# Kernel optimization log

Measured on AMD Instinct MI355X. Metric: run time of the kernel, lower is better.

The kernel has to match this reference:

```python
import jax, jax.numpy as jnp
import numpy as np
import math

B, HW, E = 128, 3136, 96
NH, WS = 3, 7
EH = E // NH
NEG_INF = float('-inf')


def setup_inputs() -> dict:
    key = jax.random.key(0)
    ks = jax.random.split(key, 5)
    x = jax.random.normal(ks[0], (B, HW, E), dtype=jnp.float32)
    w1 = jax.random.normal(ks[1], (3 * E, E), dtype=jnp.float32) * 0.02
    b1 = jnp.zeros((3 * E,), dtype=jnp.float32)
    w2 = jax.random.normal(ks[2], (E, E), dtype=jnp.float32) * 0.02
    b2 = jnp.zeros((E,), dtype=jnp.float32)
    return {"x": x, "w1": w1, "b1": b1, "w2": w2, "b2": b2}


def _masks():
    m = WS * (WS // 2)  # 21
    row = jnp.zeros((WS * WS, WS * WS), dtype=jnp.float32)
    row = row.at[-m:, :-m].set(NEG_INF)
    row = row.at[:-m, -m:].set(NEG_INF)
    # rearrange '(r w1) (c w2) -> (w1 r) (w2 c)'
    col = row.reshape(WS, WS, WS, WS).transpose(1, 0, 3, 2).reshape(WS * WS, WS * WS)
    return row, col


def reference(x, w1, b1, w2, b2):
    b = x.shape[0]
    hh = ww = int(round(math.sqrt(x.shape[1])))
    nh, nw = hh // WS, ww // WS
    qkv = x @ w1.T + b1                      # [b, hw, 3E]
    qkv = qkv.reshape(b, hh, ww, E, 3)       # (c K) split, K=3
    # cyclic shift: (-WS)//2 == -4 (faithful to torch source)
    s = (-WS) // 2
    qkv = jnp.roll(qkv, (s, s), axis=(1, 2))
    # window partition: b (h m1) (w m2) (H E) K -> b H h w (m1 m2) E K
    t = qkv.reshape(b, nh, WS, nw, WS, NH, EH, 3)
    t = t.transpose(0, 5, 1, 3, 2, 4, 6, 7).reshape(b, NH, nh, nw, WS * WS, EH, 3)
    q, k, v = t[..., 0], t[..., 1], t[..., 2]
    att = jnp.einsum('bHxyqe,bHxyke->bHxyqk', q, k) / math.sqrt(EH)
    row_mask, col_mask = _masks()
    att = att.at[:, :, -1, :].add(row_mask)
    att = att.at[:, :, :, -1].add(col_mask)
    p = jax.nn.softmax(att, axis=-1)
    o = jnp.einsum('bHxyqk,bHxyke->bHxyqe', p, v)
    # reverse window partition: b H h w (m1 m2) E -> b (h m1) (w m2) (H E)
    o = o.reshape(b, NH, nh, nw, WS, WS, EH)
    o = o.transpose(0, 2, 4, 3, 5, 1, 6).reshape(b, hh, ww, E)
    o = jnp.roll(o, (WS // 2, WS // 2), axis=(1, 2))  # +3 (faithful)
    o = o.reshape(b, hh * ww, E)
    return o @ w2.T + b2
```

## Files before the change

kernel.cpp:

```cpp
#include <hip/hip_runtime.h>

typedef __attribute__((ext_vector_type(8))) __bf16 bf16x8;
typedef __attribute__((ext_vector_type(4))) float f32x4;
typedef __attribute__((ext_vector_type(4))) unsigned int u32x4;

__device__ __forceinline__ unsigned short f2bf(float f){
    unsigned int x = __builtin_bit_cast(unsigned int, f);
    x += 0x7FFFu + ((x >> 16) & 1u);
    return (unsigned short)(x >> 16);
}
__device__ __forceinline__ unsigned int pk2(float a, float b){
    return (unsigned int)f2bf(a) | ((unsigned int)f2bf(b) << 16);
}
__device__ __forceinline__ bf16x8 ldfrag(const unsigned short* p){
    u32x4 v = *reinterpret_cast<const u32x4*>(p);
    return __builtin_bit_cast(bf16x8, v);
}
__device__ __forceinline__ bf16x8 ldf32(const float* p){
    f32x4 a = *reinterpret_cast<const f32x4*>(p);
    f32x4 b = *reinterpret_cast<const f32x4*>(p + 4);
    u32x4 r;
    r[0] = pk2(a[0], a[1]); r[1] = pk2(a[2], a[3]);
    r[2] = pk2(b[0], b[1]); r[3] = pk2(b[2], b[3]);
    return __builtin_bit_cast(bf16x8, r);
}
__device__ __forceinline__ f32x4 mfma_bf16(bf16x8 a, bf16x8 b, f32x4 c){
    return __builtin_amdgcn_mfma_f32_16x16x32_bf16(a, b, c, 0, 0, 0);
}

#define W1F_SH 27648
#define W2F_SH 9216

__global__ __launch_bounds__(256) void k_prep(const float* __restrict__ w1,
                                              const float* __restrict__ b1,
                                              const float* __restrict__ w2,
                                              unsigned short* __restrict__ w1f,
                                              unsigned short* __restrict__ w2f,
                                              float* __restrict__ b1p)
{
    int i = blockIdx.x * 256 + threadIdx.x;
    if (i < 3456){
        int f = i >> 6, lane = i & 63;
        int n = f / 3, ks = f - n * 3;
        int l15 = lane & 15, qd = lane >> 4;
        int rp = n * 16 + l15;
        int c = rp / 96, rem = rp - c * 96;
        const float* src = w1 + (size_t)(3 * rem + c) * 96 + ks * 32 + qd * 8;
        f32x4 v0 = *reinterpret_cast<const f32x4*>(src);
        f32x4 v1 = *reinterpret_cast<const f32x4*>(src + 4);
        u32x4 p;
        p[0] = pk2(v0[0], v0[1]); p[1] = pk2(v0[2], v0[3]);
        p[2] = pk2(v1[0], v1[1]); p[3] = pk2(v1[2], v1[3]);
        *reinterpret_cast<u32x4*>(w1f + (size_t)f * 512 + lane * 8) = p;
    } else if (i < 4608){
        int j = i - 3456;
        int f = j >> 6, lane = j & 63;
        int n = f / 3, ks = f - n * 3;
        int l15 = lane & 15, qd = lane >> 4;
        const float* src = w2 + (size_t)(n * 16 + l15) * 96 + ks * 32 + qd * 8;
        f32x4 v0 = *reinterpret_cast<const f32x4*>(src);
        f32x4 v1 = *reinterpret_cast<const f32x4*>(src + 4);
        u32x4 p;
        p[0] = pk2(v0[0], v0[1]); p[1] = pk2(v0[2], v0[3]);
        p[2] = pk2(v1[0], v1[1]); p[3] = pk2(v1[2], v1[3]);
        *reinterpret_cast<u32x4*>(w2f + (size_t)f * 512 + lane * 8) = p;
    } else if (i < 4896){
        int rp = i - 4608;
        int c = rp / 96, rem = rp - c * 96;
        b1p[rp] = b1[3 * rem + c];
    }
}

__global__ __launch_bounds__(256, 4) void k_fused(const float* __restrict__ x,
                                                  const unsigned short* __restrict__ w1f,
                                                  const float* __restrict__ b1p,
                                                  const unsigned short* __restrict__ w2f,
                                                  const float* __restrict__ b2,
                                                  float* __restrict__ out)
{
    __shared__ __align__(16) unsigned short smem[19200];
    unsigned short* Qr = smem;
    unsigned short* Kr = smem + 6144;
    unsigned short* Vt = smem + 12288;
    unsigned short* o_lds = smem;
    float* o2 = reinterpret_cast<float*>(smem + 6144);

    const int tid = threadIdx.x;
    const int win = blockIdx.x;
    const int b = win >> 6, wy = (win >> 3) & 7, wx = win & 7;
    const int wave = tid >> 6, lane = tid & 63;
    const int l15 = lane & 15, qd = lane >> 4;

    {
        int pos = wave * 16 + l15;
        int iy = pos / 7, ix = pos - iy * 7;
        int h = wy * 7 + iy + 4; if (h >= 56) h -= 56;
        int w = wx * 7 + ix + 4; if (w >= 56) w -= 56;
        const float* xr = x + ((size_t)b * 3136 + h * 56 + w) * 96 + qd * 8;
        bf16x8 aX0 = ldf32(xr);
        bf16x8 aX1 = ldf32(xr + 32);
        bf16x8 aX2 = ldf32(xr + 64);

        f32x4 acc[18];
#pragma unroll
        for (int n = 0; n < 18; ++n){
            const unsigned short* wf = w1f + (size_t)(n * 3) * 512 + lane * 8;
            f32x4 a = {0.f, 0.f, 0.f, 0.f};
            a = mfma_bf16(aX0, ldfrag(wf), a);
            a = mfma_bf16(aX1, ldfrag(wf + 512), a);
            a = mfma_bf16(aX2, ldfrag(wf + 1024), a);
            acc[n] = a;
        }
        float bias[18];
#pragma unroll
        for (int n = 0; n < 18; ++n) bias[n] = b1p[n * 16 + l15];

#pragma unroll
        for (int n = 0; n < 18; ++n){
            if (n < 12){
                int c = n / 6, H = (n % 6) >> 1;
                int eh = ((n & 1) << 4) + l15;
                int ch = eh >> 3;
                unsigned short* base = (c == 0 ? Qr : Kr) + H * 2048;
#pragma unroll
                for (int r = 0; r < 4; ++r){
                    int p = wave * 16 + qd * 4 + r;
                    int chs = ch ^ ((p >> 1) & 3);
                    base[p * 32 + chs * 8 + (eh & 7)] = f2bf(acc[n][r] + bias[n]);
                }
            } else {
                int H = (n - 12) >> 1;
                int eh = ((n & 1) << 4) + l15;
#pragma unroll
                for (int r = 0; r < 4; ++r){
                    int p = wave * 16 + qd * 4 + r;
                    Vt[(H * 32 + eh) * 72 + p] = f2bf(acc[n][r] + bias[n]);
                }
            }
        }
    }
    __syncthreads();

    const bool rowm = (wy == 7), colm = (wx == 7);
    const float scale = 0.17677669529663687f;
    const float NEGINF = -__builtin_inff();

    unsigned int m49 = 0, m28 = 0, m7 = 0;
#pragma unroll
    for (int tn = 0; tn < 4; ++tn)
#pragma unroll
        for (int r = 0; r < 4; ++r){
            int col = tn * 16 + qd * 4 + r;
            int bit = tn * 4 + r;
            m49 |= (unsigned)(col >= 49) << bit;
            m28 |= (unsigned)(col >= 28) << bit;
            m7  |= (unsigned)((col % 7) >= 4) << bit;
        }
    const int src0 = l15 + 16 * ((2 * qd) & 3);
    const int src1 = l15 + 16 * ((2 * qd + 1) & 3);
    const int chq = qd ^ ((l15 >> 1) & 3);

    for (int u = 0; u < 3; ++u){
        int unit = wave * 3 + u;
        int H = unit >> 2, tm = unit & 3;
        int qrow = tm * 16 + l15;
        bool rhi = (qrow >= 28);
        bool rc7 = ((qrow % 7) >= 4);

        bf16x8 bQ = ldfrag(Qr + H * 2048 + (tm * 16 + l15) * 32 + chq * 8);
        f32x4 S[4];
#pragma unroll
        for (int tn = 0; tn < 4; ++tn){
            bf16x8 aK = ldfrag(Kr + H * 2048 + (tn * 16 + l15) * 32 + chq * 8);
            f32x4 z = {0.f, 0.f, 0.f, 0.f};
            S[tn] = mfma_bf16(aK, bQ, z);
        }

        float mx = NEGINF;
#pragma unroll
        for (int tn = 0; tn < 4; ++tn)
#pragma unroll
            for (int r = 0; r < 4; ++r){
                int bit = tn * 4 + r;
                float v = S[tn][r] * scale;
                bool blocked = (((m49 >> bit) & 1u) != 0u)
                    || (rowm && (rhi != (((m28 >> bit) & 1u) != 0u)))
                    || (colm && (rc7 != (((m7 >> bit) & 1u) != 0u)));
                v = blocked ? NEGINF : v;
                S[tn][r] = v;
                mx = fmaxf(mx, v);
            }
        mx = fmaxf(mx, __shfl_xor(mx, 16, 64));
        mx = fmaxf(mx, __shfl_xor(mx, 32, 64));
        float sum = 0.f;
#pragma unroll
        for (int tn = 0; tn < 4; ++tn)
#pragma unroll
            for (int r = 0; r < 4; ++r){
                float e = exp2f((S[tn][r] - mx) * 1.4426950408889634f);
                S[tn][r] = e;
                sum += e;
            }
        sum += __shfl_xor(sum, 16, 64);
        sum += __shfl_xor(sum, 32, 64);
        float inv = 1.f / sum;

        unsigned int pkv[8];
#pragma unroll
        for (int tn = 0; tn < 4; ++tn){
            pkv[tn * 2]     = pk2(S[tn][0], S[tn][1]);
            pkv[tn * 2 + 1] = pk2(S[tn][2], S[tn][3]);
        }

        f32x4 O[2];
        O[0] = (f32x4){0.f, 0.f, 0.f, 0.f};
        O[1] = (f32x4){0.f, 0.f, 0.f, 0.f};
#pragma unroll
        for (int kt = 0; kt < 2; ++kt){
            u32x4 aw;
#pragma unroll
            for (int w4 = 0; w4 < 4; ++w4){
                int srcl = (w4 < 2) ? src0 : src1;
                unsigned int lo = (unsigned int)__shfl((int)pkv[(2 * kt) * 2 + (w4 & 1)], srcl, 64);
                unsigned int hi = (unsigned int)__shfl((int)pkv[(2 * kt + 1) * 2 + (w4 & 1)], srcl, 64);
                aw[w4] = (qd >= 2) ? hi : lo;
            }
            bf16x8 aP = __builtin_bit_cast(bf16x8, aw);
#pragma unroll
            for (int tn = 0; tn < 2; ++tn){
                bf16x8 bV = ldfrag(Vt + (H * 32 + tn * 16 + l15) * 72 + kt * 32 + qd * 8);
                O[tn] = mfma_bf16(aP, bV, O[tn]);
            }
        }

#pragma unroll
        for (int r = 0; r < 4; ++r){
            float invr = __shfl(inv, qd * 4 + r, 64);
            int p = tm * 16 + qd * 4 + r;
            int swz = (p >> 1) & 3;
#pragma unroll
            for (int tn = 0; tn < 2; ++tn){
                int eh = tn * 16 + l15;
                int chs = (eh >> 3) ^ swz;
                o_lds[(H * 64 + p) * 32 + chs * 8 + (eh & 7)] = f2bf(O[tn][r] * invr);
            }
        }
    }
    __syncthreads();

    {
        int prow = wave * 16 + l15;
        bf16x8 a0 = ldfrag(o_lds + (0 * 64 + prow) * 32 + chq * 8);
        bf16x8 a1 = ldfrag(o_lds + (1 * 64 + prow) * 32 + chq * 8);
        bf16x8 a2 = ldfrag(o_lds + (2 * 64 + prow) * 32 + chq * 8);
#pragma unroll
        for (int n = 0; n < 6; ++n){
            const unsigned short* wf = w2f + (size_t)(n * 3) * 512 + lane * 8;
            f32x4 a = {0.f, 0.f, 0.f, 0.f};
            a = mfma_bf16(a0, ldfrag(wf), a);
            a = mfma_bf16(a1, ldfrag(wf + 512), a);
            a = mfma_bf16(a2, ldfrag(wf + 1024), a);
            float bias2 = b2[n * 16 + l15];
#pragma unroll
            for (int r = 0; r < 4; ++r)
                o2[(wave * 16 + qd * 4 + r) * 100 + n * 16 + l15] = a[r] + bias2;
        }
    }
    __syncthreads();

    {
        int row = tid >> 2, seg = tid & 3;
        if (row < 49){
            int iy = row / 7, ix = row - iy * 7;
            int h = wy * 7 + iy + 3; if (h >= 56) h -= 56;
            int w = wx * 7 + ix + 3; if (w >= 56) w -= 56;
            const float* src = o2 + row * 100 + seg * 24;
            float* dst = out + ((size_t)b * 3136 + h * 56 + w) * 96 + seg * 24;
#pragma unroll
            for (int v = 0; v < 6; ++v){
                f32x4 t4;
#pragma unroll
                for (int j = 0; j < 4; ++j) t4[j] = src[v * 4 + j];
                *reinterpret_cast<f32x4*>(dst + v * 4) = t4;
            }
        }
    }
}

extern "C" void kernel_launch(void* const* d_in, const int* in_sizes, int n_in,
                              void* d_out, int out_size, void* d_ws, size_t ws_size,
                              hipStream_t stream)
{
    const float* x  = (const float*)d_in[0];
    const float* w1 = (const float*)d_in[1];
    const float* b1 = (const float*)d_in[2];
    const float* w2 = (const float*)d_in[3];
    const float* b2 = (const float*)d_in[4];
    float* out = (float*)d_out;

    unsigned short* w1f = (unsigned short*)d_ws;
    unsigned short* w2f = w1f + W1F_SH;
    float* b1p = (float*)(w2f + W2F_SH);

    hipLaunchKernelGGL(k_prep,  dim3(20),   dim3(256), 0, stream, w1, b1, w2, w1f, w2f, b1p);
    hipLaunchKernelGGL(k_fused, dim3(8192), dim3(256), 0, stream, x, w1f, b1p, w2f, b2, out);
}
```

Before: 382.3 us.

## Keep Q, P and O in registers using 16x16x16 MFMA layouts

```diff
diff --git a/kernel.cpp b/kernel.cpp
--- a/kernel.cpp
+++ b/kernel.cpp
@@ -1,8 +1,10 @@
 #include <hip/hip_runtime.h>
 
 typedef __attribute__((ext_vector_type(8))) __bf16 bf16x8;
+typedef __attribute__((ext_vector_type(4))) short short4v;
 typedef __attribute__((ext_vector_type(4))) float f32x4;
 typedef __attribute__((ext_vector_type(4))) unsigned int u32x4;
+typedef __attribute__((ext_vector_type(2))) unsigned int u32x2;
 
 __device__ __forceinline__ unsigned short f2bf(float f){
     unsigned int x = __builtin_bit_cast(unsigned int, f);
@@ -28,62 +30,98 @@
     return __builtin_amdgcn_mfma_f32_16x16x32_bf16(a, b, c, 0, 0, 0);
 }
 
-#define W1F_SH 27648
-#define W2F_SH 9216
+#if defined(__has_builtin)
+#if __has_builtin(__builtin_amdgcn_mfma_f32_16x16x16bf16_1k)
+#define HAVE_MFMA16 1
+#endif
+#endif
+__device__ __forceinline__ f32x4 mfma16(short4v a, short4v b, f32x4 c){
+#ifdef HAVE_MFMA16
+    return __builtin_amdgcn_mfma_f32_16x16x16bf16_1k(a, b, c, 0, 0, 0);
+#else
+    f32x4 d;
+    asm volatile("s_nop 1\n\tv_mfma_f32_16x16x16_bf16 %0, %1, %2, %3\n\ts_nop 7\n\ts_nop 7"
+                 : "=v"(d) : "v"(a), "v"(b), "v"(c));
+    return d;
+#endif
+}
+
+#define VSTR 72
 
 __global__ __launch_bounds__(256) void k_prep(const float* __restrict__ w1,
                                               const float* __restrict__ b1,
                                               const float* __restrict__ w2,
-                                              unsigned short* __restrict__ w1f,
-                                              unsigned short* __restrict__ w2f,
-                                              float* __restrict__ b1p)
+                                              unsigned short* __restrict__ w1k,
+                                              unsigned short* __restrict__ w1v,
+                                              unsigned short* __restrict__ w1q,
+                                              unsigned short* __restrict__ w2p,
+                                              float* __restrict__ bias3)
 {
+    const float SCALE = 0.17677669529663687f;
     int i = blockIdx.x * 256 + threadIdx.x;
-    if (i < 3456){
-        int f = i >> 6, lane = i & 63;
+    if (i < 2304){
+        int half = i / 1152;
+        int j = i - half * 1152;
+        int f = j >> 6, lane = j & 63;
         int n = f / 3, ks = f - n * 3;
         int l15 = lane & 15, qd = lane >> 4;
-        int rp = n * 16 + l15;
-        int c = rp / 96, rem = rp - c * 96;
-        const float* src = w1 + (size_t)(3 * rem + c) * 96 + ks * 32 + qd * 8;
+        int row = 3 * (n * 16 + l15) + 1 + half;
+        const float* src = w1 + (size_t)row * 96 + ks * 32 + qd * 8;
         f32x4 v0 = *reinterpret_cast<const f32x4*>(src);
         f32x4 v1 = *reinterpret_cast<const f32x4*>(src + 4);
         u32x4 p;
         p[0] = pk2(v0[0], v0[1]); p[1] = pk2(v0[2], v0[3]);
         p[2] = pk2(v1[0], v1[1]); p[3] = pk2(v1[2], v1[3]);
-        *reinterpret_cast<u32x4*>(w1f + (size_t)f * 512 + lane * 8) = p;
+        unsigned short* dst = (half ? w1v : w1k) + (size_t)f * 512 + lane * 8;
+        *reinterpret_cast<u32x4*>(dst) = p;
     } else if (i < 4608){
-        int j = i - 3456;
+        int j = i - 2304;
         int f = j >> 6, lane = j & 63;
-        int n = f / 3, ks = f - n * 3;
+        int qt = f / 6, ks = f - qt * 6;
         int l15 = lane & 15, qd = lane >> 4;
-        const float* src = w2 + (size_t)(n * 16 + l15) * 96 + ks * 32 + qd * 8;
-        f32x4 v0 = *reinterpret_cast<const f32x4*>(src);
-        f32x4 v1 = *reinterpret_cast<const f32x4*>(src + 4);
-        u32x4 p;
-        p[0] = pk2(v0[0], v0[1]); p[1] = pk2(v0[2], v0[3]);
-        p[2] = pk2(v1[0], v1[1]); p[3] = pk2(v1[2], v1[3]);
-        *reinterpret_cast<u32x4*>(w2f + (size_t)f * 512 + lane * 8) = p;
-    } else if (i < 4896){
-        int rp = i - 4608;
-        int c = rp / 96, rem = rp - c * 96;
-        b1p[rp] = b1[3 * rem + c];
+        int row = 3 * (qt * 16 + l15);
+        const float* src = w1 + (size_t)row * 96 + ks * 16 + qd * 4;
+        f32x4 v = *reinterpret_cast<const f32x4*>(src);
+        u32x2 p;
+        p[0] = pk2(v[0] * SCALE, v[1] * SCALE);
+        p[1] = pk2(v[2] * SCALE, v[3] * SCALE);
+        *reinterpret_cast<u32x2*>(w1q + (size_t)(qt * 3 + (ks >> 1)) * 512 + lane * 8 + (ks & 1) * 4) = p;
+    } else if (i < 6912){
+        int j = i - 4608;
+        int f = j >> 6, lane = j & 63;
+        int n = f / 6, ct = f - n * 6;
+        int l15 = lane & 15, qd = lane >> 4;
+        const float* src = w2 + (size_t)(n * 16 + l15) * 96 + ct * 16 + qd * 4;
+        f32x4 v = *reinterpret_cast<const f32x4*>(src);
+        u32x2 p;
+        p[0] = pk2(v[0], v[1]); p[1] = pk2(v[2], v[3]);
+        *reinterpret_cast<u32x2*>(w2p + (size_t)(n * 3 + (ct >> 1)) * 512 + lane * 8 + (ct & 1) * 4) = p;
+    } else if (i < 7200){
+        int e = i - 6912;
+        int g = e / 96, r = e - g * 96;
+        if (g == 0)      bias3[r]       = b1[3 * r + 1];
+        else if (g == 1) bias3[96 + r]  = b1[3 * r + 2];
+        else             bias3[192 + r] = b1[3 * r] * SCALE;
     }
 }
 
 __global__ __launch_bounds__(256, 4) void k_fused(const float* __restrict__ x,
-                                                  const unsigned short* __restrict__ w1f,
-                                                  const float* __restrict__ b1p,
-                                                  const unsigned short* __restrict__ w2f,
+                                                  const unsigned short* __restrict__ w1k,
+                                                  const unsigned short* __restrict__ w1v,
+                                                  const unsigned short* __restrict__ w1q,
+                                                  const unsigned short* __restrict__ w2p,
+                                                  const float* __restrict__ bias3,
                                                   const float* __restrict__ b2,
                                                   float* __restrict__ out)
 {
-    __shared__ __align__(16) unsigned short smem[19200];
-    unsigned short* Qr = smem;
-    unsigned short* Kr = smem + 6144;
-    unsigned short* Vt = smem + 12288;
-    unsigned short* o_lds = smem;
-    float* o2 = reinterpret_cast<float*>(smem + 6144);
+    __shared__ __align__(16) unsigned short smem[13056];
+    unsigned short* Kr = smem;
+    unsigned short* Vt = smem + 6144;
+    float* o2 = reinterpret_cast<float*>(smem);
+
+    const float* b1k = bias3;
+    const float* b1v = bias3 + 96;
+    const float* b1q = bias3 + 192;
 
     const int tid = threadIdx.x;
     const int win = blockIdx.x;
@@ -91,60 +129,92 @@
     const int wave = tid >> 6, lane = tid & 63;
     const int l15 = lane & 15, qd = lane >> 4;
 
+    short4v bQ[6];
     {
         int pos = wave * 16 + l15;
         int iy = pos / 7, ix = pos - iy * 7;
         int h = wy * 7 + iy + 4; if (h >= 56) h -= 56;
         int w = wx * 7 + ix + 4; if (w >= 56) w -= 56;
-        const float* xr = x + ((size_t)b * 3136 + h * 56 + w) * 96 + qd * 8;
-        bf16x8 aX0 = ldf32(xr);
-        bf16x8 aX1 = ldf32(xr + 32);
-        bf16x8 aX2 = ldf32(xr + 64);
-
-        f32x4 acc[18];
-#pragma unroll
-        for (int n = 0; n < 18; ++n){
-            const unsigned short* wf = w1f + (size_t)(n * 3) * 512 + lane * 8;
+        const float* xr = x + ((size_t)b * 3136 + h * 56 + w) * 96;
+
+        bf16x8 aX0 = ldf32(xr + qd * 8);
+        bf16x8 aX1 = ldf32(xr + 32 + qd * 8);
+        bf16x8 aX2 = ldf32(xr + 64 + qd * 8);
+        short4v bX[6];
+#pragma unroll
+        for (int ks = 0; ks < 6; ++ks){
+            f32x4 v = *reinterpret_cast<const f32x4*>(xr + ks * 16 + qd * 4);
+            u32x2 p; p[0] = pk2(v[0], v[1]); p[1] = pk2(v[2], v[3]);
+            bX[ks] = __builtin_bit_cast(short4v, p);
+        }
+
+        f32x4 acc[12];
+#pragma unroll
+        for (int n = 0; n < 6; ++n){
+            const unsigned short* wf = w1k + (size_t)(n * 3) * 512 + lane * 8;
             f32x4 a = {0.f, 0.f, 0.f, 0.f};
             a = mfma_bf16(aX0, ldfrag(wf), a);
             a = mfma_bf16(aX1, ldfrag(wf + 512), a);
             a = mfma_bf16(aX2, ldfrag(wf + 1024), a);
             acc[n] = a;
         }
-        float bias[18];
-#pragma unroll
-        for (int n = 0; n < 18; ++n) bias[n] = b1p[n * 16 + l15];
-
-#pragma unroll
-        for (int n = 0; n < 18; ++n){
-            if (n < 12){
-                int c = n / 6, H = (n % 6) >> 1;
-                int eh = ((n & 1) << 4) + l15;
-                int ch = eh >> 3;
-                unsigned short* base = (c == 0 ? Qr : Kr) + H * 2048;
-#pragma unroll
-                for (int r = 0; r < 4; ++r){
-                    int p = wave * 16 + qd * 4 + r;
-                    int chs = ch ^ ((p >> 1) & 3);
-                    base[p * 32 + chs * 8 + (eh & 7)] = f2bf(acc[n][r] + bias[n]);
-                }
-            } else {
-                int H = (n - 12) >> 1;
-                int eh = ((n & 1) << 4) + l15;
-#pragma unroll
-                for (int r = 0; r < 4; ++r){
-                    int p = wave * 16 + qd * 4 + r;
-                    Vt[(H * 32 + eh) * 72 + p] = f2bf(acc[n][r] + bias[n]);
-                }
-            }
+#pragma unroll
+        for (int n = 0; n < 6; ++n){
+            const unsigned short* wf = w1v + (size_t)(n * 3) * 512 + lane * 8;
+            f32x4 a = {0.f, 0.f, 0.f, 0.f};
+            a = mfma_bf16(aX0, ldfrag(wf), a);
+            a = mfma_bf16(aX1, ldfrag(wf + 512), a);
+            a = mfma_bf16(aX2, ldfrag(wf + 1024), a);
+            acc[6 + n] = a;
+        }
+
+#pragma unroll
+        for (int n = 0; n < 6; ++n){
+            int H = n >> 1;
+            int eh = ((n & 1) << 4) + l15;
+            int ch = eh >> 3;
+            float bb = b1k[n * 16 + l15];
+#pragma unroll
+            for (int r = 0; r < 4; ++r){
+                int p = wave * 16 + qd * 4 + r;
+                int chs = ch ^ ((p >> 1) & 3);
+                Kr[H * 2048 + p * 32 + chs * 8 + (eh & 7)] = f2bf(acc[n][r] + bb);
+            }
+        }
+#pragma unroll
+        for (int n = 0; n < 6; ++n){
+            int H = n >> 1;
+            int eh = ((n & 1) << 4) + l15;
+            float bb = b1v[n * 16 + l15];
+#pragma unroll
+            for (int r = 0; r < 4; ++r){
+                int p = wave * 16 + qd * 4 + r;
+                Vt[(H * 32 + eh) * VSTR + p] = f2bf(acc[6 + n][r] + bb);
+            }
+        }
+
+#pragma unroll
+        for (int qt = 0; qt < 6; ++qt){
+            const unsigned short* wf = w1q + (size_t)(qt * 3) * 512 + lane * 8;
+            f32x4 a = {0.f, 0.f, 0.f, 0.f};
+#pragma unroll
+            for (int p = 0; p < 3; ++p){
+                u32x4 wv = *reinterpret_cast<const u32x4*>(wf + p * 512);
+                u32x2 wl = {wv[0], wv[1]}, wh = {wv[2], wv[3]};
+                a = mfma16(__builtin_bit_cast(short4v, wl), bX[2 * p],     a);
+                a = mfma16(__builtin_bit_cast(short4v, wh), bX[2 * p + 1], a);
+            }
+            f32x4 bq = *reinterpret_cast<const f32x4*>(b1q + qt * 16 + qd * 4);
+            u32x2 pq;
+            pq[0] = pk2(a[0] + bq[0], a[1] + bq[1]);
+            pq[1] = pk2(a[2] + bq[2], a[3] + bq[3]);
+            bQ[qt] = __builtin_bit_cast(short4v, pq);
         }
     }
     __syncthreads();
 
     const bool rowm = (wy == 7), colm = (wx == 7);
-    const float scale = 0.17677669529663687f;
     const float NEGINF = -__builtin_inff();
-
     unsigned int m49 = 0, m28 = 0, m7 = 0;
 #pragma unroll
     for (int tn = 0; tn < 4; ++tn)
@@ -156,24 +226,25 @@
             m28 |= (unsigned)(col >= 28) << bit;
             m7  |= (unsigned)((col % 7) >= 4) << bit;
         }
-    const int src0 = l15 + 16 * ((2 * qd) & 3);
-    const int src1 = l15 + 16 * ((2 * qd + 1) & 3);
-    const int chq = qd ^ ((l15 >> 1) & 3);
-
-    for (int u = 0; u < 3; ++u){
-        int unit = wave * 3 + u;
-        int H = unit >> 2, tm = unit & 3;
-        int qrow = tm * 16 + l15;
-        bool rhi = (qrow >= 28);
-        bool rc7 = ((qrow % 7) >= 4);
-
-        bf16x8 bQ = ldfrag(Qr + H * 2048 + (tm * 16 + l15) * 32 + chq * 8);
+    const int qrow = wave * 16 + l15;
+    const bool rhi = (qrow >= 28);
+    const bool rc7 = ((qrow % 7) >= 4);
+
+    short4v aO[6];
+#pragma unroll
+    for (int H = 0; H < 3; ++H){
         f32x4 S[4];
 #pragma unroll
         for (int tn = 0; tn < 4; ++tn){
-            bf16x8 aK = ldfrag(Kr + H * 2048 + (tn * 16 + l15) * 32 + chq * 8);
-            f32x4 z = {0.f, 0.f, 0.f, 0.f};
-            S[tn] = mfma_bf16(aK, bQ, z);
+            f32x4 s = {0.f, 0.f, 0.f, 0.f};
+#pragma unroll
+            for (int kt = 0; kt < 2; ++kt){
+                int p = tn * 16 + l15;
+                int chs = (kt * 2 + (qd >> 1)) ^ ((p >> 1) & 3);
+                const unsigned short* ka = Kr + H * 2048 + p * 32 + chs * 8 + (qd & 1) * 4;
+                s = mfma16(*reinterpret_cast<const short4v*>(ka), bQ[H * 2 + kt], s);
+            }
+            S[tn] = s;
         }
 
         float mx = NEGINF;
@@ -182,7 +253,7 @@
 #pragma unroll
             for (int r = 0; r < 4; ++r){
                 int bit = tn * 4 + r;
-                float v = S[tn][r] * scale;
+                float v = S[tn][r];
                 bool blocked = (((m49 >> bit) & 1u) != 0u)
                     || (rowm && (rhi != (((m28 >> bit) & 1u) != 0u)))
                     || (colm && (rc7 != (((m7 >> bit) & 1u) != 0u)));
@@ -205,66 +276,52 @@
         sum += __shfl_xor(sum, 32, 64);
         float inv = 1.f / sum;
 
-        unsigned int pkv[8];
+        short4v bP[4];
 #pragma unroll
         for (int tn = 0; tn < 4; ++tn){
-            pkv[tn * 2]     = pk2(S[tn][0], S[tn][1]);
-            pkv[tn * 2 + 1] = pk2(S[tn][2], S[tn][3]);
-        }
-
-        f32x4 O[2];
-        O[0] = (f32x4){0.f, 0.f, 0.f, 0.f};
-        O[1] = (f32x4){0.f, 0.f, 0.f, 0.f};
-#pragma unroll
-        for (int kt = 0; kt < 2; ++kt){
-            u32x4 aw;
-#pragma unroll
-            for (int w4 = 0; w4 < 4; ++w4){
-                int srcl = (w4 < 2) ? src0 : src1;
-                unsigned int lo = (unsigned int)__shfl((int)pkv[(2 * kt) * 2 + (w4 & 1)], srcl, 64);
-                unsigned int hi = (unsigned int)__shfl((int)pkv[(2 * kt + 1) * 2 + (w4 & 1)], srcl, 64);
-                aw[w4] = (qd >= 2) ? hi : lo;
-            }
-            bf16x8 aP = __builtin_bit_cast(bf16x8, aw);
-#pragma unroll
-            for (int tn = 0; tn < 2; ++tn){
-                bf16x8 bV = ldfrag(Vt + (H * 32 + tn * 16 + l15) * 72 + kt * 32 + qd * 8);
-                O[tn] = mfma_bf16(aP, bV, O[tn]);
-            }
-        }
-
-#pragma unroll
-        for (int r = 0; r < 4; ++r){
-            float invr = __shfl(inv, qd * 4 + r, 64);
-            int p = tm * 16 + qd * 4 + r;
-            int swz = (p >> 1) & 3;
-#pragma unroll
-            for (int tn = 0; tn < 2; ++tn){
-                int eh = tn * 16 + l15;
-                int chs = (eh >> 3) ^ swz;
-                o_lds[(H * 64 + p) * 32 + chs * 8 + (eh & 7)] = f2bf(O[tn][r] * invr);
-            }
-        }
+            u32x2 pp;
+            pp[0] = pk2(S[tn][0], S[tn][1]);
+            pp[1] = pk2(S[tn][2], S[tn][3]);
+            bP[tn] = __builtin_bit_cast(short4v, pp);
+        }
+
+#pragma unroll
+        for (int et = 0; et < 2; ++et){
+            f32x4 o = {0.f, 0.f, 0.f, 0.f};
+#pragma unroll
+            for (int kt4 = 0; kt4 < 4; ++kt4){
+                const unsigned short* va = Vt + (H * 32 + et * 16 + l15) * VSTR + kt4 * 16 + qd * 4;
+                o = mfma16(*reinterpret_cast<const short4v*>(va), bP[kt4], o);
+            }
+            u32x2 po;
+            po[0] = pk2(o[0] * inv, o[1] * inv);
+            po[1] = pk2(o[2] * inv, o[3] * inv);
+            aO[H * 2 + et] = __builtin_bit_cast(short4v, po);
+        }
+    }
+
+    f32x4 acc2[6];
+#pragma unroll
+    for (int n = 0; n < 6; ++n){
+        const unsigned short* wf = w2p + (size_t)(n * 3) * 512 + lane * 8;
+        f32x4 a = {0.f, 0.f, 0.f, 0.f};
+#pragma unroll
+        for (int p = 0; p < 3; ++p){
+            u32x4 wv = *reinterpret_cast<const u32x4*>(wf + p * 512);
+            u32x2 wl = {wv[0], wv[1]}, wh = {wv[2], wv[3]};
+            a = mfma16(aO[2 * p],     __builtin_bit_cast(short4v, wl), a);
+            a = mfma16(aO[2 * p + 1], __builtin_bit_cast(short4v, wh), a);
+        }
+        acc2[n] = a;
     }
     __syncthreads();
 
-    {
-        int prow = wave * 16 + l15;
-        bf16x8 a0 = ldfrag(o_lds + (0 * 64 + prow) * 32 + chq * 8);
-        bf16x8 a1 = ldfrag(o_lds + (1 * 64 + prow) * 32 + chq * 8);
-        bf16x8 a2 = ldfrag(o_lds + (2 * 64 + prow) * 32 + chq * 8);
-#pragma unroll
-        for (int n = 0; n < 6; ++n){
-            const unsigned short* wf = w2f + (size_t)(n * 3) * 512 + lane * 8;
-            f32x4 a = {0.f, 0.f, 0.f, 0.f};
-            a = mfma_bf16(a0, ldfrag(wf), a);
-            a = mfma_bf16(a1, ldfrag(wf + 512), a);
-            a = mfma_bf16(a2, ldfrag(wf + 1024), a);
-            float bias2 = b2[n * 16 + l15];
-#pragma unroll
-            for (int r = 0; r < 4; ++r)
-                o2[(wave * 16 + qd * 4 + r) * 100 + n * 16 + l15] = a[r] + bias2;
-        }
+#pragma unroll
+    for (int n = 0; n < 6; ++n){
+        float bb = b2[n * 16 + l15];
+#pragma unroll
+        for (int r = 0; r < 4; ++r)
+            o2[(wave * 16 + qd * 4 + r) * 100 + n * 16 + l15] = acc2[n][r] + bb;
     }
     __syncthreads();
 
@@ -298,10 +355,12 @@
     const float* b2 = (const float*)d_in[4];
     float* out = (float*)d_out;
 
-    unsigned short* w1f = (unsigned short*)d_ws;
-    unsigned short* w2f = w1f + W1F_SH;
-    float* b1p = (float*)(w2f + W2F_SH);
-
-    hipLaunchKernelGGL(k_prep,  dim3(20),   dim3(256), 0, stream, w1, b1, w2, w1f, w2f, b1p);
-    hipLaunchKernelGGL(k_fused, dim3(8192), dim3(256), 0, stream, x, w1f, b1p, w2f, b2, out);
-}
+    unsigned short* w1k = (unsigned short*)d_ws;
+    unsigned short* w1v = w1k + 9216;
+    unsigned short* w1q = w1k + 18432;
+    unsigned short* w2p = w1k + 27648;
+    float* bias3 = (float*)(w1k + 36864);
+
+    hipLaunchKernelGGL(k_prep,  dim3(29),   dim3(256), 0, stream, w1, b1, w2, w1k, w1v, w1q, w2p, bias3);
+    hipLaunchKernelGGL(k_fused, dim3(8192), dim3(256), 0, stream, x, w1k, w1v, w1q, w2p, bias3, b2, out);
+}
```

Result: no change. 389.0 us (+1.8%).

## Keep Q and attention output in registers via lane shuffles, fold scale into weights

Applied to the files above, without the earlier changes.

```diff
diff --git a/kernel.cpp b/kernel.cpp
--- a/kernel.cpp
+++ b/kernel.cpp
@@ -38,6 +38,7 @@
                                               unsigned short* __restrict__ w2f,
                                               float* __restrict__ b1p)
 {
+    const float SCALE = 0.17677669529663687f;
     int i = blockIdx.x * 256 + threadIdx.x;
     if (i < 3456){
         int f = i >> 6, lane = i & 63;
@@ -45,12 +46,13 @@
         int l15 = lane & 15, qd = lane >> 4;
         int rp = n * 16 + l15;
         int c = rp / 96, rem = rp - c * 96;
+        float s = (c == 0) ? SCALE : 1.0f;
         const float* src = w1 + (size_t)(3 * rem + c) * 96 + ks * 32 + qd * 8;
         f32x4 v0 = *reinterpret_cast<const f32x4*>(src);
         f32x4 v1 = *reinterpret_cast<const f32x4*>(src + 4);
         u32x4 p;
-        p[0] = pk2(v0[0], v0[1]); p[1] = pk2(v0[2], v0[3]);
-        p[2] = pk2(v1[0], v1[1]); p[3] = pk2(v1[2], v1[3]);
+        p[0] = pk2(v0[0] * s, v0[1] * s); p[1] = pk2(v0[2] * s, v0[3] * s);
+        p[2] = pk2(v1[0] * s, v1[1] * s); p[3] = pk2(v1[2] * s, v1[3] * s);
         *reinterpret_cast<u32x4*>(w1f + (size_t)f * 512 + lane * 8) = p;
     } else if (i < 4608){
         int j = i - 3456;
@@ -67,84 +69,106 @@
     } else if (i < 4896){
         int rp = i - 4608;
         int c = rp / 96, rem = rp - c * 96;
-        b1p[rp] = b1[3 * rem + c];
-    }
-}
-
-__global__ __launch_bounds__(256, 4) void k_fused(const float* __restrict__ x,
+        b1p[rp] = b1[3 * rem + c] * ((c == 0) ? SCALE : 1.0f);
+    }
+}
+
+__global__ __launch_bounds__(256, 5) void k_fused(const float* __restrict__ x,
                                                   const unsigned short* __restrict__ w1f,
                                                   const float* __restrict__ b1p,
                                                   const unsigned short* __restrict__ w2f,
                                                   const float* __restrict__ b2,
                                                   float* __restrict__ out)
 {
-    __shared__ __align__(16) unsigned short smem[19200];
-    unsigned short* Qr = smem;
-    unsigned short* Kr = smem + 6144;
-    unsigned short* Vt = smem + 12288;
-    unsigned short* o_lds = smem;
-    float* o2 = reinterpret_cast<float*>(smem + 6144);
+    __shared__ __align__(16) unsigned short smem[13056];
+    unsigned short* Kr = smem;
+    unsigned short* Vt = smem + 6144;
+    float* o2 = reinterpret_cast<float*>(smem);
 
     const int tid = threadIdx.x;
     const int win = blockIdx.x;
     const int b = win >> 6, wy = (win >> 3) & 7, wx = win & 7;
     const int wave = tid >> 6, lane = tid & 63;
     const int l15 = lane & 15, qd = lane >> 4;
-
+    const int s0 = (qd & 1) * 32 + l15;
+    const int s1 = s0 + 16;
+
+    bf16x8 bQf[3];
     {
         int pos = wave * 16 + l15;
         int iy = pos / 7, ix = pos - iy * 7;
         int h = wy * 7 + iy + 4; if (h >= 56) h -= 56;
         int w = wx * 7 + ix + 4; if (w >= 56) w -= 56;
-        const float* xr = x + ((size_t)b * 3136 + h * 56 + w) * 96 + qd * 8;
-        bf16x8 aX0 = ldf32(xr);
-        bf16x8 aX1 = ldf32(xr + 32);
-        bf16x8 aX2 = ldf32(xr + 64);
-
-        f32x4 acc[18];
-#pragma unroll
-        for (int n = 0; n < 18; ++n){
-            const unsigned short* wf = w1f + (size_t)(n * 3) * 512 + lane * 8;
+        const float* xr = x + ((size_t)b * 3136 + h * 56 + w) * 96;
+        bf16x8 aX0 = ldf32(xr + qd * 8);
+        bf16x8 aX1 = ldf32(xr + 32 + qd * 8);
+        bf16x8 aX2 = ldf32(xr + 64 + qd * 8);
+
+        unsigned int Qw[12];
+#pragma unroll
+        for (int qt = 0; qt < 6; ++qt){
+            const unsigned short* wf = w1f + (size_t)(qt * 3) * 512 + lane * 8;
             f32x4 a = {0.f, 0.f, 0.f, 0.f};
-            a = mfma_bf16(aX0, ldfrag(wf), a);
-            a = mfma_bf16(aX1, ldfrag(wf + 512), a);
+            a = mfma_bf16(ldfrag(wf),        aX0, a);
+            a = mfma_bf16(ldfrag(wf + 512),  aX1, a);
+            a = mfma_bf16(ldfrag(wf + 1024), aX2, a);
+            f32x4 bq = *reinterpret_cast<const f32x4*>(b1p + qt * 16 + qd * 4);
+            Qw[qt * 2]     = pk2(a[0] + bq[0], a[1] + bq[1]);
+            Qw[qt * 2 + 1] = pk2(a[2] + bq[2], a[3] + bq[3]);
+        }
+#pragma unroll
+        for (int H = 0; H < 3; ++H){
+            u32x4 qw; unsigned int lo, hi;
+            lo = (unsigned)__shfl((int)Qw[(2*H)*2],     s0, 64);
+            hi = (unsigned)__shfl((int)Qw[(2*H+1)*2],   s0, 64); qw[0] = (qd & 2) ? hi : lo;
+            lo = (unsigned)__shfl((int)Qw[(2*H)*2+1],   s0, 64);
+            hi = (unsigned)__shfl((int)Qw[(2*H+1)*2+1], s0, 64); qw[1] = (qd & 2) ? hi : lo;
+            lo = (unsigned)__shfl((int)Qw[(2*H)*2],     s1, 64);
+            hi = (unsigned)__shfl((int)Qw[(2*H+1)*2],   s1, 64); qw[2] = (qd & 2) ? hi : lo;
+            lo = (unsigned)__shfl((int)Qw[(2*H)*2+1],   s1, 64);
+            hi = (unsigned)__shfl((int)Qw[(2*H+1)*2+1], s1, 64); qw[3] = (qd & 2) ? hi : lo;
+            bQf[H] = __builtin_bit_cast(bf16x8, qw);
+        }
+
+#pragma unroll
+        for (int n = 0; n < 6; ++n){
+            const unsigned short* wf = w1f + (size_t)((6 + n) * 3) * 512 + lane * 8;
+            f32x4 a = {0.f, 0.f, 0.f, 0.f};
+            a = mfma_bf16(aX0, ldfrag(wf),        a);
+            a = mfma_bf16(aX1, ldfrag(wf + 512),  a);
             a = mfma_bf16(aX2, ldfrag(wf + 1024), a);
-            acc[n] = a;
-        }
-        float bias[18];
-#pragma unroll
-        for (int n = 0; n < 18; ++n) bias[n] = b1p[n * 16 + l15];
-
-#pragma unroll
-        for (int n = 0; n < 18; ++n){
-            if (n < 12){
-                int c = n / 6, H = (n % 6) >> 1;
-                int eh = ((n & 1) << 4) + l15;
-                int ch = eh >> 3;
-                unsigned short* base = (c == 0 ? Qr : Kr) + H * 2048;
-#pragma unroll
-                for (int r = 0; r < 4; ++r){
-                    int p = wave * 16 + qd * 4 + r;
-                    int chs = ch ^ ((p >> 1) & 3);
-                    base[p * 32 + chs * 8 + (eh & 7)] = f2bf(acc[n][r] + bias[n]);
-                }
-            } else {
-                int H = (n - 12) >> 1;
-                int eh = ((n & 1) << 4) + l15;
-#pragma unroll
-                for (int r = 0; r < 4; ++r){
-                    int p = wave * 16 + qd * 4 + r;
-                    Vt[(H * 32 + eh) * 72 + p] = f2bf(acc[n][r] + bias[n]);
-                }
+            float bb = b1p[(6 + n) * 16 + l15];
+            int H = n >> 1;
+            int eh = ((n & 1) << 4) + l15;
+            int ch = eh >> 3;
+#pragma unroll
+            for (int r = 0; r < 4; ++r){
+                int p = wave * 16 + qd * 4 + r;
+                int chs = ch ^ ((p >> 1) & 3);
+                Kr[H * 2048 + p * 32 + chs * 8 + (eh & 7)] = f2bf(a[r] + bb);
+            }
+        }
+#pragma unroll
+        for (int n = 0; n < 6; ++n){
+            const unsigned short* wf = w1f + (size_t)((12 + n) * 3) * 512 + lane * 8;
+            f32x4 a = {0.f, 0.f, 0.f, 0.f};
+            a = mfma_bf16(aX0, ldfrag(wf),        a);
+            a = mfma_bf16(aX1, ldfrag(wf + 512),  a);
+            a = mfma_bf16(aX2, ldfrag(wf + 1024), a);
+            float bb = b1p[(12 + n) * 16 + l15];
+            int H = n >> 1;
+            int eh = ((n & 1) << 4) + l15;
+#pragma unroll
+            for (int r = 0; r < 4; ++r){
+                int p = wave * 16 + qd * 4 + r;
+                Vt[(H * 32 + eh) * 72 + p] = f2bf(a[r] + bb);
             }
         }
     }
     __syncthreads();
 
     const bool rowm = (wy == 7), colm = (wx == 7);
-    const float scale = 0.17677669529663687f;
     const float NEGINF = -__builtin_inff();
-
     unsigned int m49 = 0, m28 = 0, m7 = 0;
 #pragma unroll
     for (int tn = 0; tn < 4; ++tn)
@@ -156,33 +180,28 @@
             m28 |= (unsigned)(col >= 28) << bit;
             m7  |= (unsigned)((col % 7) >= 4) << bit;
         }
-    const int src0 = l15 + 16 * ((2 * qd) & 3);
-    const int src1 = l15 + 16 * ((2 * qd + 1) & 3);
+    const int qrow = wave * 16 + l15;
+    const bool rhi = (qrow >= 28);
+    const bool rc7 = ((qrow % 7) >= 4);
     const int chq = qd ^ ((l15 >> 1) & 3);
 
-    for (int u = 0; u < 3; ++u){
-        int unit = wave * 3 + u;
-        int H = unit >> 2, tm = unit & 3;
-        int qrow = tm * 16 + l15;
-        bool rhi = (qrow >= 28);
-        bool rc7 = ((qrow % 7) >= 4);
-
-        bf16x8 bQ = ldfrag(Qr + H * 2048 + (tm * 16 + l15) * 32 + chq * 8);
+    unsigned int Ow[12];
+#pragma unroll
+    for (int H = 0; H < 3; ++H){
         f32x4 S[4];
 #pragma unroll
         for (int tn = 0; tn < 4; ++tn){
             bf16x8 aK = ldfrag(Kr + H * 2048 + (tn * 16 + l15) * 32 + chq * 8);
             f32x4 z = {0.f, 0.f, 0.f, 0.f};
-            S[tn] = mfma_bf16(aK, bQ, z);
-        }
-
+            S[tn] = mfma_bf16(aK, bQf[H], z);
+        }
         float mx = NEGINF;
 #pragma unroll
         for (int tn = 0; tn < 4; ++tn)
 #pragma unroll
             for (int r = 0; r < 4; ++r){
                 int bit = tn * 4 + r;
-                float v = S[tn][r] * scale;
+                float v = S[tn][r];
                 bool blocked = (((m49 >> bit) & 1u) != 0u)
                     || (rowm && (rhi != (((m28 >> bit) & 1u) != 0u)))
                     || (colm && (rc7 != (((m7 >> bit) & 1u) != 0u)));
@@ -211,60 +230,65 @@
             pkv[tn * 2]     = pk2(S[tn][0], S[tn][1]);
             pkv[tn * 2 + 1] = pk2(S[tn][2], S[tn][3]);
         }
-
-        f32x4 O[2];
-        O[0] = (f32x4){0.f, 0.f, 0.f, 0.f};
-        O[1] = (f32x4){0.f, 0.f, 0.f, 0.f};
+        bf16x8 pF[2];
 #pragma unroll
         for (int kt = 0; kt < 2; ++kt){
             u32x4 aw;
 #pragma unroll
             for (int w4 = 0; w4 < 4; ++w4){
-                int srcl = (w4 < 2) ? src0 : src1;
-                unsigned int lo = (unsigned int)__shfl((int)pkv[(2 * kt) * 2 + (w4 & 1)], srcl, 64);
-                unsigned int hi = (unsigned int)__shfl((int)pkv[(2 * kt + 1) * 2 + (w4 & 1)], srcl, 64);
-                aw[w4] = (qd >= 2) ? hi : lo;
-            }
-            bf16x8 aP = __builtin_bit_cast(bf16x8, aw);
-#pragma unroll
-            for (int tn = 0; tn < 2; ++tn){
-                bf16x8 bV = ldfrag(Vt + (H * 32 + tn * 16 + l15) * 72 + kt * 32 + qd * 8);
-                O[tn] = mfma_bf16(aP, bV, O[tn]);
-            }
-        }
-
-#pragma unroll
-        for (int r = 0; r < 4; ++r){
-            float invr = __shfl(inv, qd * 4 + r, 64);
-            int p = tm * 16 + qd * 4 + r;
-            int swz = (p >> 1) & 3;
-#pragma unroll
-            for (int tn = 0; tn < 2; ++tn){
-                int eh = tn * 16 + l15;
-                int chs = (eh >> 3) ^ swz;
-                o_lds[(H * 64 + p) * 32 + chs * 8 + (eh & 7)] = f2bf(O[tn][r] * invr);
-            }
-        }
+                int srcl = (w4 < 2) ? s0 : s1;
+                unsigned int lo = (unsigned)__shfl((int)pkv[(2 * kt) * 2 + (w4 & 1)], srcl, 64);
+                unsigned int hi = (unsigned)__shfl((int)pkv[(2 * kt + 1) * 2 + (w4 & 1)], srcl, 64);
+                aw[w4] = (qd & 2) ? hi : lo;
+            }
+            pF[kt] = __builtin_bit_cast(bf16x8, aw);
+        }
+#pragma unroll
+        for (int et = 0; et < 2; ++et){
+            f32x4 o = {0.f, 0.f, 0.f, 0.f};
+#pragma unroll
+            for (int kt = 0; kt < 2; ++kt){
+                bf16x8 aV = ldfrag(Vt + (H * 32 + et * 16 + l15) * 72 + kt * 32 + qd * 8);
+                o = mfma_bf16(aV, pF[kt], o);
+            }
+            Ow[(H * 2 + et) * 2]     = pk2(o[0] * inv, o[1] * inv);
+            Ow[(H * 2 + et) * 2 + 1] = pk2(o[2] * inv, o[3] * inv);
+        }
+    }
+
+    bf16x8 aO[3];
+#pragma unroll
+    for (int c = 0; c < 3; ++c){
+        u32x4 qw; unsigned int lo, hi;
+        lo = (unsigned)__shfl((int)Ow[(2*c)*2],     s0, 64);
+        hi = (unsigned)__shfl((int)Ow[(2*c+1)*2],   s0, 64); qw[0] = (qd & 2) ? hi : lo;
+        lo = (unsigned)__shfl((int)Ow[(2*c)*2+1],   s0, 64);
+        hi = (unsigned)__shfl((int)Ow[(2*c+1)*2+1], s0, 64); qw[1] = (qd & 2) ? hi : lo;
+        lo = (unsigned)__shfl((int)Ow[(2*c)*2],     s1, 64);
+        hi = (unsigned)__shfl((int)Ow[(2*c+1)*2],   s1, 64); qw[2] = (qd & 2) ? hi : lo;
+        lo = (unsigned)__shfl((int)Ow[(2*c)*2+1],   s1, 64);
+        hi = (unsigned)__shfl((int)Ow[(2*c+1)*2+1], s1, 64); qw[3] = (qd & 2) ? hi : lo;
+        aO[c] = __builtin_bit_cast(bf16x8, qw);
+    }
+
+    f32x4 acc2[6];
+#pragma unroll
+    for (int n = 0; n < 6; ++n){
+        const unsigned short* wf = w2f + (size_t)(n * 3) * 512 + lane * 8;
+        f32x4 a = {0.f, 0.f, 0.f, 0.f};
+        a = mfma_bf16(aO[0], ldfrag(wf),        a);
+        a = mfma_bf16(aO[1], ldfrag(wf + 512),  a);
+        a = mfma_bf16(aO[2], ldfrag(wf + 1024), a);
+        acc2[n] = a;
     }
     __syncthreads();
 
-    {
-        int prow = wave * 16 + l15;
-        bf16x8 a0 = ldfrag(o_lds + (0 * 64 + prow) * 32 + chq * 8);
-        bf16x8 a1 = ldfrag(o_lds + (1 * 64 + prow) * 32 + chq * 8);
-        bf16x8 a2 = ldfrag(o_lds + (2 * 64 + prow) * 32 + chq * 8);
-#pragma unroll
-        for (int n = 0; n < 6; ++n){
-            const unsigned short* wf = w2f + (size_t)(n * 3) * 512 + lane * 8;
-            f32x4 a = {0.f, 0.f, 0.f, 0.f};
-            a = mfma_bf16(a0, ldfrag(wf), a);
-            a = mfma_bf16(a1, ldfrag(wf + 512), a);
-            a = mfma_bf16(a2, ldfrag(wf + 1024), a);
-            float bias2 = b2[n * 16 + l15];
-#pragma unroll
-            for (int r = 0; r < 4; ++r)
-                o2[(wave * 16 + qd * 4 + r) * 100 + n * 16 + l15] = a[r] + bias2;
-        }
+#pragma unroll
+    for (int n = 0; n < 6; ++n){
+        float bb = b2[n * 16 + l15];
+#pragma unroll
+        for (int r = 0; r < 4; ++r)
+            o2[(wave * 16 + qd * 4 + r) * 100 + n * 16 + l15] = acc2[n][r] + bb;
     }
     __syncthreads();
 
```

New measurement: 393.3 us. +2.9%, slower.
